# Optimization experiments

Measured on AMD Instinct MI355X. Metric: run time of the kernel, lower is better.

The kernel has to match this reference:

```python
import jax, jax.numpy as jnp
import numpy as np
from jax.scipy.special import erf

# ---- physical constants (scipy.constants values; FIELD_CONSTANT in eV*Angstrom per e^2) ----
E_CHARGE = 1.602176634e-19
EPS0 = 8.8541878128e-12
PI = float(np.pi)
FIELD_CONSTANT = E_CHARGE * 1e10 / EPS0          # e/(eps0) with Angstrom length units
K_COUL = FIELD_CONSTANT / (4.0 * PI)             # ~14.3996 eV*A

# ---- module hyperparameters (from init_kwargs) ----
SIGMA_D = 0.5
SIGMAS = np.array([0.4, 0.8, 1.2, 1.6], dtype=np.float32)
NUM_RADIAL = 4
OFFSET = 0.1
N_PER_GRAPH = 128
NUM_GRAPHS = 32
M_NODES = N_PER_GRAPH * NUM_GRAPHS

# total_width_factors = sqrt((sigma_d^2 + sigma_r^2)/2)
W_FACTORS = np.sqrt((SIGMA_D**2 + SIGMAS**2) / 2.0).astype(np.float32)      # [R]
# multipole-normalized GTO: C_l = 1/(2^{l+1/2} sigma^{2l+3} Gamma(l+3/2)) => C1/C0 = 1/(3 sigma^2)
L0_FACTORS = np.ones(NUM_RADIAL, dtype=np.float32)                          # ratio = 1 under 'multipoles'
L1_FACTORS = (np.sqrt(3.0) * SIGMAS**2 * (1.0 / (3.0 * SIGMAS**2)) / OFFSET).astype(np.float32)

# 7 duplicate offsets: center, +x, +y, +z, -x, -y, -z
_h = OFFSET
OFFSETS7 = np.array([[0,0,0],[_h,0,0],[0,_h,0],[0,0,_h],[-_h,0,0],[0,-_h,0],[0,0,-_h]], dtype=np.float32)


def _duplicate_charges(sf):
    # sf: [M,4] -> [M,7] FD charge assignment (matches torch slot layout)
    t = 2.0 * OFFSET
    s0, s1, s2, s3 = sf[:, 0], sf[:, 1], sf[:, 2], sf[:, 3]
    return jnp.stack([s0, s3 / t, s1 / t, s2 / t, -s3 / t, -s1 / t, -s2 / t], axis=1)


def _project(sf7):
    # sf7: [M,7,R] per-duplicate scalar features -> [M, 4R]
    M = sf7.shape[0]
    l0 = jnp.asarray(L0_FACTORS) * sf7[:, 0]                                 # [M,R]
    half = 0.5 * jnp.asarray(L1_FACTORS)
    vy = half * (sf7[:, 2] - sf7[:, 5])   # column offset 0 in each triplet
    vz = half * (sf7[:, 3] - sf7[:, 6])   # column offset 1
    vx = half * (sf7[:, 1] - sf7[:, 4])   # column offset 2
    l1 = jnp.stack([vy, vz, vx], axis=-1).reshape(M, 3 * NUM_RADIAL)         # interleaved per radial
    return jnp.concatenate([l0, l1], axis=1)                                 # [M,4R]


def setup_inputs() -> dict:
    key = jax.random.key(0)
    k1, k2 = jax.random.split(key)
    source_feats = jax.random.normal(k1, (M_NODES, 1, 4), dtype=jnp.float32)
    node_positions = 4.0 * jax.random.normal(k2, (M_NODES, 3), dtype=jnp.float32)  # ~Angstrom scale
    batch = jnp.repeat(jnp.arange(NUM_GRAPHS, dtype=jnp.int64), N_PER_GRAPH)
    return {"source_feats": source_feats, "node_positions": node_positions, "batch": batch}


def reference(source_feats, node_positions, batch):
    # density_max_l=1, projection_max_l=1 -> call_density_1_feats_1 path.
    # Assumes equal-size graphs: batch = repeat(arange(G), n) (enforced by setup_inputs).
    sf = source_feats[:, 0, :]                                               # squeeze(-2): [M,4]
    M = sf.shape[0]
    G, n, D, R = NUM_GRAPHS, N_PER_GRAPH, 7 * N_PER_GRAPH, NUM_RADIAL
    w = jnp.asarray(W_FACTORS)                                               # [R]

    charges = _duplicate_charges(sf)                                         # [M,7]
    pos7 = node_positions[:, None, :] + jnp.asarray(OFFSETS7)[None]          # [M,7,3]

    pg = pos7.reshape(G, D, 3)
    cg = charges.reshape(G, D)

    diff = pg[:, :, None, :] - pg[:, None, :, :]                             # [G,D,D,3]
    d2 = jnp.sum(diff * diff, axis=-1)                                       # [G,D,D]
    orig = jnp.arange(D) // 7
    mask = (orig[:, None] != orig[None, :])                                  # exclude same-original-node pairs
    d = jnp.sqrt(jnp.where(mask, d2, 1.0))                                   # safe sqrt (masked entries dummy)
    smooth = erf(0.5 * d[..., None] / w) / (d[..., None] + 1e-6)             # [G,D,D,R]
    smooth = smooth * mask[None, :, :, None]
    # scatter_sum over senders i into receivers j
    sfeat = K_COUL * jnp.einsum('gi,gijr->gjr', cg, smooth)                  # [G,D,R]
    sfeat = sfeat.reshape(M, 7, R)

    # GTOSelfInteractionBlock (reconstructed): interactions among a node's own
    # 7 duplicates with analytic d->0 limit erf(x)/x -> 1/(w*sqrt(pi)).
    off = jnp.asarray(OFFSETS7)
    ds = jnp.linalg.norm(off[:, None, :] - off[None, :, :], axis=-1)          # [7,7]
    phi = jnp.where(ds[..., None] > 0.0,
                    erf(0.5 * ds[..., None] / w) / (ds[..., None] + 1e-6),
                    1.0 / (w * np.sqrt(PI)))                                  # [7,7,R]
    sself = K_COUL * jnp.einsum('mi,ijr->mjr', charges, phi)                  # [M,7,R]

    features = _project(sfeat)
    self_terms = _project(sself)
    features = features + self_terms                                          # include_self_interaction=True
    return features, self_terms
```

## Files before the change

kernel.cpp:

```cpp
#include <hip/hip_runtime.h>
#include <math.h>

namespace {

constexpr int   MTOT = 4096;
constexpr float H    = 0.1f;

constexpr float W0 = 0.45276925690687087f;
constexpr float W1 = 0.66708320320631664f;
constexpr float W2 = 0.91923881554251174f;
constexpr float W3 = 1.18532695911296985f;

constexpr float KCOUL   = 14.399645478425669f;
constexpr float HALF_L1 = 2.8867513459481287f;
constexpr float SQRTPI  = 1.7724538509055159f;

constexpr float PK0 = 0.5195472f, PK1 = 0.3526314f, PK2 = 0.2559019f, PK3 = 0.1984558f;
constexpr float C20 = -1.7593842f, C21 = -0.8105028f, C22 = -0.4268329f, C23 = -0.2567073f;
constexpr float EA1 = 0.3480242f, EA2 = -0.0958798f, EA3 = 0.7478556f;
constexpr float RCP_H = 9.9999000f, RCP_HS2 = 7.0710178f, RCP_2H = 4.9999750f;

constexpr float KQ0 = -0.24921720f, KQ1 = -0.16915128f, KQ2 = -0.12275067f, KQ3 = -0.09519549f;

constexpr float NEAR2 = 4.0f;
constexpr float SAT2  = 49.4f;

__device__ __forceinline__ float fast_rcp(float x)  { return __builtin_amdgcn_rcpf(x); }
__device__ __forceinline__ float fast_rsq(float x)  { return __builtin_amdgcn_rsqf(x); }
__device__ __forceinline__ float fast_exp2(float x) { return __builtin_amdgcn_exp2f(x); }

__device__ __forceinline__ float erf_q(float d, float d2, float pk, float c2) {
  float t = fast_rcp(__builtin_fmaf(d, pk, 1.0f));
  float poly = t * __builtin_fmaf(t, __builtin_fmaf(t, EA3, EA2), EA1);
  return poly * fast_exp2(d2 * c2);
}

__device__ __forceinline__ float project_one(const float* S, int k) {
  if (k < 4) return S[k];
  int q = k - 4;
  int r = q / 3;
  int comp = q - 3 * r;
  int j1, j2;
  if (comp == 0)      { j1 = 2; j2 = 5; }
  else if (comp == 1) { j1 = 3; j2 = 6; }
  else                { j1 = 1; j2 = 4; }
  return HALF_L1 * (S[j1 * 4 + r] - S[j2 * 4 + r]);
}

__device__ __forceinline__ unsigned spread3(int v) {
  return (unsigned)((v & 1) | ((v & 2) << 2) | ((v & 4) << 4));
}

__global__ __launch_bounds__(896, 4) void es_main(
    const float* __restrict__ sf,
    const float* __restrict__ pos,
    float* __restrict__ out)
{
  __shared__ float4   s_pos4[128];
  __shared__ float4   s_chg4[128];
  __shared__ int      s_orig[128];
  __shared__ unsigned s_key[128];
  __shared__ float4   s_part[8 * 112];
  __shared__ float    s_feat[448];
  __shared__ float    s_self[448];

  const int b   = blockIdx.x;
  const int g   = b >> 3;
  const int nb  = b & 7;
  const int tid = threadIdx.x;

  float px = 0.f, py = 0.f, pz = 0.f;
  float4 myc = make_float4(0.f, 0.f, 0.f, 0.f);
  if (tid < 128) {
    const float* p = pos + (size_t)(g * 128 + tid) * 3;
    px = p[0]; py = p[1]; pz = p[2];
    const float4 s = ((const float4*)sf)[g * 128 + tid];
    myc = make_float4(s.x, 5.0f * s.w, 5.0f * s.y, 5.0f * s.z);
    int cx = (int)((px + 16.0f) * 0.25f); cx = (cx < 0) ? 0 : (cx > 7 ? 7 : cx);
    int cy = (int)((py + 16.0f) * 0.25f); cy = (cy < 0) ? 0 : (cy > 7 ? 7 : cy);
    int cz = (int)((pz + 16.0f) * 0.25f); cz = (cz < 0) ? 0 : (cz > 7 ? 7 : cz);
    unsigned mort = spread3(cx) | (spread3(cy) << 1) | (spread3(cz) << 2);
    s_key[tid] = (mort << 7) | (unsigned)tid;
  }
  __syncthreads();

  if (tid < 128) {
    const unsigned mykey = s_key[tid];
    int rank = 0;
    for (int t = 0; t < 128; ++t) rank += (s_key[t] < mykey) ? 1 : 0;
    s_pos4[rank] = make_float4(px, py, pz, 0.0f);
    s_chg4[rank] = myc;
    s_orig[rank] = tid;
  }
  __syncthreads();

  const int site_local = tid % 112;
  const int chunk      = tid / 112;
  const int sl   = nb * 112 + site_local;
  const int jown = (sl * 9363) >> 16;
  const int aoff = sl - jown * 7;

  const float4 cp = s_pos4[jown];
  const float tx = cp.x + ((aoff == 1) ? H : (aoff == 4) ? -H : 0.0f);
  const float ty = cp.y + ((aoff == 2) ? H : (aoff == 5) ? -H : 0.0f);
  const float tz = cp.z + ((aoff == 3) ? H : (aoff == 6) ? -H : 0.0f);

  float a0 = 0.f, a1 = 0.f, a2 = 0.f, a3 = 0.f, Ssat = 0.f;

  auto acc_full = [&](float d2raw, float c) {
    const float d2 = fmaxf(d2raw, 1e-12f);
    const float rd = fast_rsq(d2);
    const float d  = d2 * rd;
    const float cv = c * rd;
    const float t0 = fast_rcp(__builtin_fmaf(d, PK0, 1.0f));
    const float t1 = fast_rcp(__builtin_fmaf(d, PK1, 1.0f));
    const float t2 = fast_rcp(__builtin_fmaf(d, PK2, 1.0f));
    const float t3 = fast_rcp(__builtin_fmaf(d, PK3, 1.0f));
    const float q0 = t0 * __builtin_fmaf(t0, __builtin_fmaf(t0, EA3, EA2), EA1) * fast_exp2(d2 * C20);
    const float q1 = t1 * __builtin_fmaf(t1, __builtin_fmaf(t1, EA3, EA2), EA1) * fast_exp2(d2 * C21);
    const float q2 = t2 * __builtin_fmaf(t2, __builtin_fmaf(t2, EA3, EA2), EA1) * fast_exp2(d2 * C22);
    const float q3 = t3 * __builtin_fmaf(t3, __builtin_fmaf(t3, EA3, EA2), EA1) * fast_exp2(d2 * C23);
    a0 = __builtin_fmaf(cv, 1.0f - q0, a0);
    a1 = __builtin_fmaf(cv, 1.0f - q1, a1);
    a2 = __builtin_fmaf(cv, 1.0f - q2, a2);
    a3 = __builtin_fmaf(cv, 1.0f - q3, a3);
  };

  const int j0 = chunk * 16;
  for (int jj = 0; jj < 16; ++jj) {
    const int j = j0 + jj;
    const float4 p4 = s_pos4[j];
    const float4 c4 = s_chg4[j];
    const float vx = tx - p4.x;
    const float vy = ty - p4.y;
    const float vz = tz - p4.z;
    const float v2 = __builtin_fmaf(vx, vx, __builtin_fmaf(vy, vy, vz * vz));
    if (__any(v2 < NEAR2)) {
      const float w2 = v2 + 0.01f;
      const bool own = (j == jown);
      acc_full(v2,                            (own & (aoff == 0)) ? 0.0f :  c4.x);
      acc_full(__builtin_fmaf(vx, -0.2f, w2), (own & (aoff == 1)) ? 0.0f :  c4.y);
      acc_full(__builtin_fmaf(vy, -0.2f, w2), (own & (aoff == 2)) ? 0.0f :  c4.z);
      acc_full(__builtin_fmaf(vz, -0.2f, w2), (own & (aoff == 3)) ? 0.0f :  c4.w);
      acc_full(__builtin_fmaf(vx,  0.2f, w2), (own & (aoff == 4)) ? 0.0f : -c4.y);
      acc_full(__builtin_fmaf(vy,  0.2f, w2), (own & (aoff == 5)) ? 0.0f : -c4.z);
      acc_full(__builtin_fmaf(vz,  0.2f, w2), (own & (aoff == 6)) ? 0.0f : -c4.w);
    } else if (__any(v2 < SAT2)) {
      const float rd  = fast_rsq(v2);
      const float d   = v2 * rd;
      const float dot = __builtin_fmaf(c4.y, vx, __builtin_fmaf(c4.z, vy, c4.w * vz));
      const float rd2 = rd * rd;
      const float P   = rd * __builtin_fmaf(0.2f * dot, rd2, c4.x);
      const float Qc  = dot * rd2;
      const float t0 = fast_rcp(__builtin_fmaf(d, PK0, 1.0f));
      const float t1 = fast_rcp(__builtin_fmaf(d, PK1, 1.0f));
      const float t2 = fast_rcp(__builtin_fmaf(d, PK2, 1.0f));
      const float t3 = fast_rcp(__builtin_fmaf(d, PK3, 1.0f));
      const float x0 = fast_exp2(v2 * C20);
      const float x1 = fast_exp2(v2 * C21);
      const float x2 = fast_exp2(v2 * C22);
      const float x3 = fast_exp2(v2 * C23);
      const float q0 = t0 * __builtin_fmaf(t0, __builtin_fmaf(t0, EA3, EA2), EA1) * x0;
      const float q1 = t1 * __builtin_fmaf(t1, __builtin_fmaf(t1, EA3, EA2), EA1) * x1;
      const float q2 = t2 * __builtin_fmaf(t2, __builtin_fmaf(t2, EA3, EA2), EA1) * x2;
      const float q3 = t3 * __builtin_fmaf(t3, __builtin_fmaf(t3, EA3, EA2), EA1) * x3;
      a0 = __builtin_fmaf(KQ0 * x0, Qc, __builtin_fmaf(-q0, P, a0 + P));
      a1 = __builtin_fmaf(KQ1 * x1, Qc, __builtin_fmaf(-q1, P, a1 + P));
      a2 = __builtin_fmaf(KQ2 * x2, Qc, __builtin_fmaf(-q2, P, a2 + P));
      a3 = __builtin_fmaf(KQ3 * x3, Qc, __builtin_fmaf(-q3, P, a3 + P));
    } else {
      const float rd  = fast_rsq(v2);
      const float dot = __builtin_fmaf(c4.y, vx, __builtin_fmaf(c4.z, vy, c4.w * vz));
      Ssat = __builtin_fmaf(c4.x, rd, Ssat);
      Ssat = __builtin_fmaf(0.2f * dot, rd * rd * rd, Ssat);
    }
  }
  a0 += Ssat; a1 += Ssat; a2 += Ssat; a3 += Ssat;

  s_part[chunk * 112 + site_local] = make_float4(a0, a1, a2, a3);
  __syncthreads();

  if (tid < 448) {
    const int site = tid >> 2;
    const int r    = tid & 3;
    const float* pf = (const float*)s_part;
    float tot = 0.f;
#pragma unroll
    for (int c = 0; c < 8; ++c) tot += pf[c * 448 + tid];

    const float w  = (r == 0) ? W0  : (r == 1) ? W1  : (r == 2) ? W2  : W3;
    const float pk = (r == 0) ? PK0 : (r == 1) ? PK1 : (r == 2) ? PK2 : PK3;
    const float c2 = (r == 0) ? C20 : (r == 1) ? C21 : (r == 2) ? C22 : C23;
    const float diag = fast_rcp(w * SQRTPI);
    const float ph1 = (1.f - erf_q(0.1f,        0.01f, pk, c2)) * RCP_H;
    const float ph2 = (1.f - erf_q(0.14142136f, 0.02f, pk, c2)) * RCP_HS2;
    const float ph3 = (1.f - erf_q(0.2f,        0.04f, pk, c2)) * RCP_2H;

    const int jn = (site * 9363) >> 16;
    const int ba = site - jn * 7;
    const float4 c4 = s_chg4[nb * 16 + jn];
    float selfSum = 0.f, ca = 0.f;
#pragma unroll
    for (int i = 0; i < 7; ++i) {
      const float ci = (i == 0) ?  c4.x : (i == 1) ?  c4.y : (i == 2) ?  c4.z :
                       (i == 3) ?  c4.w : (i == 4) ? -c4.y : (i == 5) ? -c4.z : -c4.w;
      float ph;
      if (i == ba)                             ph = diag;
      else if (i == 0 || ba == 0)              ph = ph1;
      else if ((i - ba == 3) || (ba - i == 3)) ph = ph3;
      else                                     ph = ph2;
      selfSum = __builtin_fmaf(ci, ph, selfSum);
      if (i == ba) ca = ci;
    }
    s_self[tid] = KCOUL * selfSum;
    s_feat[tid] = KCOUL * __builtin_fmaf(ca, diag, tot);
  }
  __syncthreads();

  if (tid < 256) {
    const int node = tid >> 4;
    const int k    = tid & 15;
    const int m    = g * 128 + s_orig[nb * 16 + node];
    float vf = project_one(&s_feat[node * 28], k);
    float vs = project_one(&s_self[node * 28], k);
    out[m * 16 + k]             = vf;
    out[MTOT * 16 + m * 16 + k] = vs;
  }
}

}

extern "C" void kernel_launch(void* const* d_in, const int* in_sizes, int n_in,
                              void* d_out, int out_size, void* d_ws, size_t ws_size,
                              hipStream_t stream) {
  const float* sf  = (const float*)d_in[0];
  const float* pos = (const float*)d_in[1];
  float* out = (float*)d_out;
  es_main<<<256, 896, 0, stream>>>(sf, pos, out);
}
```

Measured before the change: 74.96 us.

## Use per-node Taylor expansion for far pairs and compact near-pair list

Replaces per-duplicate-site evaluation with one wave per target node. Far source nodes contribute through an analytic potential plus gradient, and that gradient is extrapolated to the six offset duplicates. Pairs within the near radius go into a shared-memory list and are evaluated exactly over all 7x7 duplicate pairs, one lane per pair. The Morton sort is dropped and the grid becomes 1024 blocks of 256 threads. The aim is to cut the seven-fold per-site erf work. The cost is a truncation error from the first-order expansion and a list capped at 256 entries.

```diff
diff --git a/kernel.cpp b/kernel.cpp
--- a/kernel.cpp
+++ b/kernel.cpp
@@ -2,6 +2,7 @@
 #include <math.h>
 
 namespace {
+
 
 constexpr int   MTOT = 4096;
 constexpr float H    = 0.1f;
@@ -15,15 +16,16 @@
 constexpr float HALF_L1 = 2.8867513459481287f;
 constexpr float SQRTPI  = 1.7724538509055159f;
 
-constexpr float PK0 = 0.5195472f, PK1 = 0.3526314f, PK2 = 0.2559019f, PK3 = 0.1984558f;
-constexpr float C20 = -1.7593842f, C21 = -0.8105028f, C22 = -0.4268329f, C23 = -0.2567073f;
+constexpr float PK[4] = {0.5195472f, 0.3526314f, 0.2559019f, 0.1984558f};
+constexpr float C2[4] = {-1.7593842f, -0.8105028f, -0.4268329f, -0.2567073f};
 constexpr float EA1 = 0.3480242f, EA2 = -0.0958798f, EA3 = 0.7478556f;
 constexpr float RCP_H = 9.9999000f, RCP_HS2 = 7.0710178f, RCP_2H = 4.9999750f;
 
-constexpr float KQ0 = -0.24921720f, KQ1 = -0.16915128f, KQ2 = -0.12275067f, KQ3 = -0.09519549f;
-
-constexpr float NEAR2 = 4.0f;
-constexpr float SAT2  = 49.4f;
+constexpr float KA[4]  = {1.2460860f, 0.84575637f, 0.61375334f, 0.47597746f};
+constexpr float K2X[4] = {2.4390243f, 1.1235959f, 0.59171598f, 0.35587189f};
+
+constexpr float NEAR2   = 6.25f;
+constexpr int   NEARCAP = 256;
 
 __device__ __forceinline__ float fast_rcp(float x)  { return __builtin_amdgcn_rcpf(x); }
 __device__ __forceinline__ float fast_rsq(float x)  { return __builtin_amdgcn_rsqf(x); }
@@ -47,184 +49,203 @@
   return HALF_L1 * (S[j1 * 4 + r] - S[j2 * 4 + r]);
 }
 
-__device__ __forceinline__ unsigned spread3(int v) {
-  return (unsigned)((v & 1) | ((v & 2) << 2) | ((v & 4) << 4));
-}
-
-__global__ __launch_bounds__(896, 4) void es_main(
+__device__ __forceinline__ float offx(int a) { return (a == 1) ? H : (a == 4) ? -H : 0.0f; }
+__device__ __forceinline__ float offy(int a) { return (a == 2) ? H : (a == 5) ? -H : 0.0f; }
+__device__ __forceinline__ float offz(int a) { return (a == 3) ? H : (a == 6) ? -H : 0.0f; }
+
+__global__ __launch_bounds__(256, 4) void es_main(
     const float* __restrict__ sf,
     const float* __restrict__ pos,
     float* __restrict__ out)
 {
-  __shared__ float4   s_pos4[128];
-  __shared__ float4   s_chg4[128];
-  __shared__ int      s_orig[128];
-  __shared__ unsigned s_key[128];
-  __shared__ float4   s_part[8 * 112];
-  __shared__ float    s_feat[448];
-  __shared__ float    s_self[448];
+  __shared__ float4 s_pos4[128];
+  __shared__ float4 s_chg4[128];
+  __shared__ float  s_red[4][16];
+  __shared__ float  s_nearS[4][7][4];
+  __shared__ int    s_nearI[NEARCAP];
+  __shared__ int    s_ncnt;
+  __shared__ float  s_feat[4 * 28];
+  __shared__ float  s_self[4 * 28];
 
   const int b   = blockIdx.x;
-  const int g   = b >> 3;
-  const int nb  = b & 7;
+  const int g   = b >> 5;
+  const int grp = b & 31;
   const int tid = threadIdx.x;
-
-  float px = 0.f, py = 0.f, pz = 0.f;
-  float4 myc = make_float4(0.f, 0.f, 0.f, 0.f);
+  const int t   = tid >> 6;
+  const int c   = tid & 63;
+
   if (tid < 128) {
     const float* p = pos + (size_t)(g * 128 + tid) * 3;
-    px = p[0]; py = p[1]; pz = p[2];
     const float4 s = ((const float4*)sf)[g * 128 + tid];
-    myc = make_float4(s.x, 5.0f * s.w, 5.0f * s.y, 5.0f * s.z);
-    int cx = (int)((px + 16.0f) * 0.25f); cx = (cx < 0) ? 0 : (cx > 7 ? 7 : cx);
-    int cy = (int)((py + 16.0f) * 0.25f); cy = (cy < 0) ? 0 : (cy > 7 ? 7 : cy);
-    int cz = (int)((pz + 16.0f) * 0.25f); cz = (cz < 0) ? 0 : (cz > 7 ? 7 : cz);
-    unsigned mort = spread3(cx) | (spread3(cy) << 1) | (spread3(cz) << 2);
-    s_key[tid] = (mort << 7) | (unsigned)tid;
-  }
-  __syncthreads();
-
-  if (tid < 128) {
-    const unsigned mykey = s_key[tid];
-    int rank = 0;
-    for (int t = 0; t < 128; ++t) rank += (s_key[t] < mykey) ? 1 : 0;
-    s_pos4[rank] = make_float4(px, py, pz, 0.0f);
-    s_chg4[rank] = myc;
-    s_orig[rank] = tid;
-  }
-  __syncthreads();
-
-  const int site_local = tid % 112;
-  const int chunk      = tid / 112;
-  const int sl   = nb * 112 + site_local;
-  const int jown = (sl * 9363) >> 16;
-  const int aoff = sl - jown * 7;
-
-  const float4 cp = s_pos4[jown];
-  const float tx = cp.x + ((aoff == 1) ? H : (aoff == 4) ? -H : 0.0f);
-  const float ty = cp.y + ((aoff == 2) ? H : (aoff == 5) ? -H : 0.0f);
-  const float tz = cp.z + ((aoff == 3) ? H : (aoff == 6) ? -H : 0.0f);
-
-  float a0 = 0.f, a1 = 0.f, a2 = 0.f, a3 = 0.f, Ssat = 0.f;
-
-  auto acc_full = [&](float d2raw, float c) {
-    const float d2 = fmaxf(d2raw, 1e-12f);
+    s_pos4[tid] = make_float4(p[0], p[1], p[2], 0.0f);
+    s_chg4[tid] = make_float4(s.x, 5.0f * s.w, 5.0f * s.y, 5.0f * s.z);
+  }
+  if (tid < 112) ((float*)s_nearS)[tid] = 0.0f;
+  if (tid == 0) s_ncnt = 0;
+  __syncthreads();
+
+  const int own = grp * 4 + t;
+  const float4 cp = s_pos4[own];
+
+  float acc[16];
+#pragma unroll
+  for (int k = 0; k < 16; ++k) acc[k] = 0.0f;
+
+#pragma unroll
+  for (int si = 0; si < 2; ++si) {
+    const int j = c + 64 * si;
+    if (j != own) {
+      const float4 p4 = s_pos4[j];
+      const float4 c4 = s_chg4[j];
+      const float vx = cp.x - p4.x;
+      const float vy = cp.y - p4.y;
+      const float vz = cp.z - p4.z;
+      const float d2 = __builtin_fmaf(vx, vx, __builtin_fmaf(vy, vy, vz * vz));
+      if (d2 < NEAR2) {
+        int slot = atomicAdd(&s_ncnt, 1);
+        if (slot < NEARCAP) s_nearI[slot] = (t << 8) | j;
+      } else {
+        const float rd  = fast_rsq(d2);
+        const float d   = d2 * rd;
+        const float rd2 = rd * rd;
+        const float rd3 = rd2 * rd;
+        const float rd4 = rd2 * rd2;
+        const float S3  = 3.0f * rd3;
+        const float S4  = 3.0f * rd4;
+        const float dot = __builtin_fmaf(c4.y, vx, __builtin_fmaf(c4.z, vy, c4.w * vz));
+        const float dp  = 0.2f * dot;
+        const float c0  = c4.x;
+#pragma unroll
+        for (int r = 0; r < 4; ++r) {
+          const float tt = fast_rcp(__builtin_fmaf(d, PK[r], 1.0f));
+          const float X  = fast_exp2(d2 * C2[r]);
+          const float q  = tt * __builtin_fmaf(tt, __builtin_fmaf(tt, EA3, EA2), EA1) * X;
+          const float E  = 1.0f - q;
+          const float A  = KA[r] * X;
+          const float gv = E * rd;
+          const float gp = (A - gv) * rd;
+          const float Bv = -gp * rd;
+          const float h1 = __builtin_fmaf(K2X[r], rd, S3);
+          const float Bp = __builtin_fmaf(A, h1, -(E * S4));
+          acc[r] = __builtin_fmaf(dp, Bv, __builtin_fmaf(c0, gv, acc[r]));
+          const float sv  = __builtin_fmaf(dp, Bp, c0 * gp) * rd;
+          const float B02 = 0.2f * Bv;
+          acc[4 + r]  = __builtin_fmaf(sv, vx, __builtin_fmaf(B02, c4.y, acc[4 + r]));
+          acc[8 + r]  = __builtin_fmaf(sv, vy, __builtin_fmaf(B02, c4.z, acc[8 + r]));
+          acc[12 + r] = __builtin_fmaf(sv, vz, __builtin_fmaf(B02, c4.w, acc[12 + r]));
+        }
+      }
+    }
+  }
+
+#pragma unroll
+  for (int k = 0; k < 16; ++k) {
+    float v = acc[k];
+    v += __shfl_xor(v, 1);
+    v += __shfl_xor(v, 2);
+    v += __shfl_xor(v, 4);
+    v += __shfl_xor(v, 8);
+    v += __shfl_xor(v, 16);
+    v += __shfl_xor(v, 32);
+    acc[k] = v;
+  }
+  if (c == 0) {
+#pragma unroll
+    for (int k = 0; k < 16; ++k) s_red[t][k] = acc[k];
+  }
+  __syncthreads();
+
+  const int N = (s_ncnt < NEARCAP) ? s_ncnt : NEARCAP;
+  for (int e = t; e < N; e += 4) {
+    const int ent = s_nearI[e];
+    const int tt  = ent >> 8;
+    const int j   = ent & 127;
+    const int a   = c >> 3;
+    const int i   = c & 7;
+    const bool act = (a < 7) && (i < 7);
+    const float4 tp = s_pos4[grp * 4 + tt];
+    const float4 p4 = s_pos4[j];
+    const float4 c4 = s_chg4[j];
+    const float ci = !act ? 0.0f :
+                     (i == 0) ?  c4.x : (i == 1) ?  c4.y : (i == 2) ?  c4.z :
+                     (i == 3) ?  c4.w : (i == 4) ? -c4.y : (i == 5) ? -c4.z : -c4.w;
+    const float sx = tp.x - p4.x + offx(a) - offx(i);
+    const float sy = tp.y - p4.y + offy(a) - offy(i);
+    const float sz = tp.z - p4.z + offz(a) - offz(i);
+    const float d2 = fmaxf(__builtin_fmaf(sx, sx, __builtin_fmaf(sy, sy, sz * sz)), 1e-12f);
     const float rd = fast_rsq(d2);
     const float d  = d2 * rd;
-    const float cv = c * rd;
-    const float t0 = fast_rcp(__builtin_fmaf(d, PK0, 1.0f));
-    const float t1 = fast_rcp(__builtin_fmaf(d, PK1, 1.0f));
-    const float t2 = fast_rcp(__builtin_fmaf(d, PK2, 1.0f));
-    const float t3 = fast_rcp(__builtin_fmaf(d, PK3, 1.0f));
-    const float q0 = t0 * __builtin_fmaf(t0, __builtin_fmaf(t0, EA3, EA2), EA1) * fast_exp2(d2 * C20);
-    const float q1 = t1 * __builtin_fmaf(t1, __builtin_fmaf(t1, EA3, EA2), EA1) * fast_exp2(d2 * C21);
-    const float q2 = t2 * __builtin_fmaf(t2, __builtin_fmaf(t2, EA3, EA2), EA1) * fast_exp2(d2 * C22);
-    const float q3 = t3 * __builtin_fmaf(t3, __builtin_fmaf(t3, EA3, EA2), EA1) * fast_exp2(d2 * C23);
-    a0 = __builtin_fmaf(cv, 1.0f - q0, a0);
-    a1 = __builtin_fmaf(cv, 1.0f - q1, a1);
-    a2 = __builtin_fmaf(cv, 1.0f - q2, a2);
-    a3 = __builtin_fmaf(cv, 1.0f - q3, a3);
-  };
-
-  const int j0 = chunk * 16;
-  for (int jj = 0; jj < 16; ++jj) {
-    const int j = j0 + jj;
-    const float4 p4 = s_pos4[j];
-    const float4 c4 = s_chg4[j];
-    const float vx = tx - p4.x;
-    const float vy = ty - p4.y;
-    const float vz = tz - p4.z;
-    const float v2 = __builtin_fmaf(vx, vx, __builtin_fmaf(vy, vy, vz * vz));
-    if (__any(v2 < NEAR2)) {
-      const float w2 = v2 + 0.01f;
-      const bool own = (j == jown);
-      acc_full(v2,                            (own & (aoff == 0)) ? 0.0f :  c4.x);
-      acc_full(__builtin_fmaf(vx, -0.2f, w2), (own & (aoff == 1)) ? 0.0f :  c4.y);
-      acc_full(__builtin_fmaf(vy, -0.2f, w2), (own & (aoff == 2)) ? 0.0f :  c4.z);
-      acc_full(__builtin_fmaf(vz, -0.2f, w2), (own & (aoff == 3)) ? 0.0f :  c4.w);
-      acc_full(__builtin_fmaf(vx,  0.2f, w2), (own & (aoff == 4)) ? 0.0f : -c4.y);
-      acc_full(__builtin_fmaf(vy,  0.2f, w2), (own & (aoff == 5)) ? 0.0f : -c4.z);
-      acc_full(__builtin_fmaf(vz,  0.2f, w2), (own & (aoff == 6)) ? 0.0f : -c4.w);
-    } else if (__any(v2 < SAT2)) {
-      const float rd  = fast_rsq(v2);
-      const float d   = v2 * rd;
-      const float dot = __builtin_fmaf(c4.y, vx, __builtin_fmaf(c4.z, vy, c4.w * vz));
-      const float rd2 = rd * rd;
-      const float P   = rd * __builtin_fmaf(0.2f * dot, rd2, c4.x);
-      const float Qc  = dot * rd2;
-      const float t0 = fast_rcp(__builtin_fmaf(d, PK0, 1.0f));
-      const float t1 = fast_rcp(__builtin_fmaf(d, PK1, 1.0f));
-      const float t2 = fast_rcp(__builtin_fmaf(d, PK2, 1.0f));
-      const float t3 = fast_rcp(__builtin_fmaf(d, PK3, 1.0f));
-      const float x0 = fast_exp2(v2 * C20);
-      const float x1 = fast_exp2(v2 * C21);
-      const float x2 = fast_exp2(v2 * C22);
-      const float x3 = fast_exp2(v2 * C23);
-      const float q0 = t0 * __builtin_fmaf(t0, __builtin_fmaf(t0, EA3, EA2), EA1) * x0;
-      const float q1 = t1 * __builtin_fmaf(t1, __builtin_fmaf(t1, EA3, EA2), EA1) * x1;
-      const float q2 = t2 * __builtin_fmaf(t2, __builtin_fmaf(t2, EA3, EA2), EA1) * x2;
-      const float q3 = t3 * __builtin_fmaf(t3, __builtin_fmaf(t3, EA3, EA2), EA1) * x3;
-      a0 = __builtin_fmaf(KQ0 * x0, Qc, __builtin_fmaf(-q0, P, a0 + P));
-      a1 = __builtin_fmaf(KQ1 * x1, Qc, __builtin_fmaf(-q1, P, a1 + P));
-      a2 = __builtin_fmaf(KQ2 * x2, Qc, __builtin_fmaf(-q2, P, a2 + P));
-      a3 = __builtin_fmaf(KQ3 * x3, Qc, __builtin_fmaf(-q3, P, a3 + P));
-    } else {
-      const float rd  = fast_rsq(v2);
-      const float dot = __builtin_fmaf(c4.y, vx, __builtin_fmaf(c4.z, vy, c4.w * vz));
-      Ssat = __builtin_fmaf(c4.x, rd, Ssat);
-      Ssat = __builtin_fmaf(0.2f * dot, rd * rd * rd, Ssat);
-    }
-  }
-  a0 += Ssat; a1 += Ssat; a2 += Ssat; a3 += Ssat;
-
-  s_part[chunk * 112 + site_local] = make_float4(a0, a1, a2, a3);
-  __syncthreads();
-
-  if (tid < 448) {
-    const int site = tid >> 2;
-    const int r    = tid & 3;
-    const float* pf = (const float*)s_part;
-    float tot = 0.f;
-#pragma unroll
-    for (int c = 0; c < 8; ++c) tot += pf[c * 448 + tid];
-
-    const float w  = (r == 0) ? W0  : (r == 1) ? W1  : (r == 2) ? W2  : W3;
-    const float pk = (r == 0) ? PK0 : (r == 1) ? PK1 : (r == 2) ? PK2 : PK3;
-    const float c2 = (r == 0) ? C20 : (r == 1) ? C21 : (r == 2) ? C22 : C23;
+    const float cv = ci * rd;
+    float vr[4];
+#pragma unroll
+    for (int r = 0; r < 4; ++r) {
+      const float tt2 = fast_rcp(__builtin_fmaf(d, PK[r], 1.0f));
+      const float q   = tt2 * __builtin_fmaf(tt2, __builtin_fmaf(tt2, EA3, EA2), EA1)
+                            * fast_exp2(d2 * C2[r]);
+      vr[r] = cv * (1.0f - q);
+    }
+#pragma unroll
+    for (int r = 0; r < 4; ++r) {
+      float v = vr[r];
+      v += __shfl_xor(v, 1);
+      v += __shfl_xor(v, 2);
+      v += __shfl_xor(v, 4);
+      vr[r] = v;
+    }
+    if (i == 0 && a < 7) {
+#pragma unroll
+      for (int r = 0; r < 4; ++r) atomicAdd(&s_nearS[tt][a][r], vr[r]);
+    }
+  }
+  __syncthreads();
+
+  if (tid < 112) {
+    const int node = tid / 28;
+    const int rem  = tid - node * 28;
+    const int a    = rem >> 2;
+    const int r    = rem & 3;
+
+    const float pot = s_red[node][r];
+    const float gx  = s_red[node][4 + r];
+    const float gy  = s_red[node][8 + r];
+    const float gz  = s_red[node][12 + r];
+    const float od  = (a == 1) ?  H * gx : (a == 2) ?  H * gy : (a == 3) ?  H * gz :
+                      (a == 4) ? -H * gx : (a == 5) ? -H * gy : (a == 6) ? -H * gz : 0.0f;
+    const float mid = pot + od + s_nearS[node][a][r];
+
+    const float w  = (r == 0) ? W0 : (r == 1) ? W1 : (r == 2) ? W2 : W3;
+    const float pk = PK[r];
+    const float c2 = C2[r];
     const float diag = fast_rcp(w * SQRTPI);
     const float ph1 = (1.f - erf_q(0.1f,        0.01f, pk, c2)) * RCP_H;
     const float ph2 = (1.f - erf_q(0.14142136f, 0.02f, pk, c2)) * RCP_HS2;
     const float ph3 = (1.f - erf_q(0.2f,        0.04f, pk, c2)) * RCP_2H;
 
-    const int jn = (site * 9363) >> 16;
-    const int ba = site - jn * 7;
-    const float4 c4 = s_chg4[nb * 16 + jn];
-    float selfSum = 0.f, ca = 0.f;
+    const float4 c4 = s_chg4[grp * 4 + node];
+    float selfSum = 0.f;
 #pragma unroll
     for (int i = 0; i < 7; ++i) {
       const float ci = (i == 0) ?  c4.x : (i == 1) ?  c4.y : (i == 2) ?  c4.z :
                        (i == 3) ?  c4.w : (i == 4) ? -c4.y : (i == 5) ? -c4.z : -c4.w;
       float ph;
-      if (i == ba)                             ph = diag;
-      else if (i == 0 || ba == 0)              ph = ph1;
-      else if ((i - ba == 3) || (ba - i == 3)) ph = ph3;
-      else                                     ph = ph2;
+      if (i == a)                            ph = diag;
+      else if (i == 0 || a == 0)             ph = ph1;
+      else if ((i - a == 3) || (a - i == 3)) ph = ph3;
+      else                                   ph = ph2;
       selfSum = __builtin_fmaf(ci, ph, selfSum);
-      if (i == ba) ca = ci;
-    }
-    s_self[tid] = KCOUL * selfSum;
-    s_feat[tid] = KCOUL * __builtin_fmaf(ca, diag, tot);
-  }
-  __syncthreads();
-
-  if (tid < 256) {
+    }
+    const float sv = KCOUL * selfSum;
+    s_self[tid] = sv;
+    s_feat[tid] = __builtin_fmaf(KCOUL, mid, sv);
+  }
+  __syncthreads();
+
+  if (tid < 64) {
     const int node = tid >> 4;
     const int k    = tid & 15;
-    const int m    = g * 128 + s_orig[nb * 16 + node];
-    float vf = project_one(&s_feat[node * 28], k);
-    float vs = project_one(&s_self[node * 28], k);
-    out[m * 16 + k]             = vf;
-    out[MTOT * 16 + m * 16 + k] = vs;
+    const int m    = g * 128 + grp * 4 + node;
+    out[m * 16 + k]             = project_one(&s_feat[node * 28], k);
+    out[MTOT * 16 + m * 16 + k] = project_one(&s_self[node * 28], k);
   }
 }
 
@@ -236,5 +257,5 @@
   const float* sf  = (const float*)d_in[0];
   const float* pos = (const float*)d_in[1];
   float* out = (float*)d_out;
-  es_main<<<256, 896, 0, stream>>>(sf, pos, out);
-}
+  es_main<<<1024, 256, 0, stream>>>(sf, pos, out);
+}
```

Measured after the change: 69.55 us. 1.08x faster.
